# Kernel tuning notes

Hardware: AMD Instinct MI355X
Metric: run time of the kernel (lower is better)

Reference implementation:

```python
import jax, jax.numpy as jnp
import numpy as np

NUM_HEAD = 8   # in_channels // 64 for in_channels=512
DIM = 8        # per-head dim (== num_head in this module)
H_CH = NUM_HEAD * DIM  # 64
SCALE = DIM ** (-0.5)


def _conv(x, w, b, padding):
    # x: [N,C,H,W], w: [O,I,kh,kw]
    out = jax.lax.conv_general_dilated(
        x, w, window_strides=(1, 1), padding=padding,
        dimension_numbers=("NCHW", "OIHW", "NCHW"))
    return out + b[None, :, None, None]


def setup_inputs() -> dict:
    key = jax.random.key(0)
    ks = jax.random.split(key, 4)
    N, C, H, W = 4, 512, 48, 48
    x = jax.random.normal(ks[0], (N, C, H, W), dtype=jnp.float32)
    qkv_w = jax.random.normal(ks[1], (3 * H_CH, C, 1, 1), dtype=jnp.float32) * 0.05
    qkv_b = jnp.zeros((3 * H_CH,), dtype=jnp.float32)
    pos_w = jax.random.normal(ks[2], (H_CH, H_CH, 3, 3), dtype=jnp.float32) * 0.05
    pos_b = jnp.zeros((H_CH,), dtype=jnp.float32)
    res_w = jax.random.normal(ks[3], (C, H_CH, 1, 1), dtype=jnp.float32) * 0.05
    res_b = jnp.zeros((C,), dtype=jnp.float32)
    return {"x": x, "qkv_w": qkv_w, "qkv_b": qkv_b,
            "pos_w": pos_w, "pos_b": pos_b,
            "res_w": res_w, "res_b": res_b}


def reference(x, qkv_w, qkv_b, pos_w, pos_b, res_w, res_b):
    N, C, H, W = x.shape
    L = H * W
    # 1x1 conv QKV projection -> [N, 3h, H, W]
    qkv = _conv(x, qkv_w, qkv_b, "VALID")
    # [N, num_head, 3*dim, L]
    qkv = qkv.reshape(N, NUM_HEAD, 3 * DIM, L)
    q, k, v = qkv[:, :, :DIM], qkv[:, :, DIM:2 * DIM], qkv[:, :, 2 * DIM:]
    # attn = q^T @ k * scale : [N, nh, L, L], softmax over keys (last dim)
    attn = jnp.einsum("nhdq,nhdk->nhqk", q, k) * SCALE
    attn = jax.nn.softmax(attn, axis=-1)
    # out = v @ attn^T : [N, nh, dim, L]
    out = jnp.einsum("nhdk,nhqk->nhdq", v, attn)
    out = out.reshape(N, H_CH, H, W)
    # positional branch: 3x3 conv on v
    pos = _conv(v.reshape(N, H_CH, H, W), pos_w, pos_b, "SAME")
    out = out + pos
    # resume 1x1 conv -> [N, out_channels, H, W]
    return _conv(out, res_w, res_b, "VALID")
```

## Files before the change

kernel.cpp:

```cpp
#include <hip/hip_runtime.h>

#define L_ATT 2304
#define QSCALE_LOG2E 0.5100695712f

using bh8 = __attribute__((ext_vector_type(8))) short;
using f4  = __attribute__((ext_vector_type(4))) float;

#if __has_builtin(__builtin_amdgcn_exp2f)
#define EXP2(x) __builtin_amdgcn_exp2f(x)
#else
#define EXP2(x) exp2f(x)
#endif

__device__ inline short f2b(float f) {
    union { float f; unsigned u; } c; c.f = f;
    unsigned r = (c.u + 0x7FFFu + ((c.u >> 16) & 1u)) >> 16;
    return (short)r;
}
__device__ inline float b2f(short s) {
    union { unsigned u; float f; } c;
    c.u = ((unsigned)(unsigned short)s) << 16;
    return c.f;
}
__device__ inline int packhi(float lo, float hi) {
    return (int)__builtin_amdgcn_perm(__float_as_uint(hi), __float_as_uint(lo), 0x07060302u);
}

__global__ __launch_bounds__(256) void prep_kernel(
    const float* __restrict__ x, const float* __restrict__ qkv_w,
    const float* __restrict__ res_w, const float* __restrict__ pos_w,
    short* __restrict__ xt, short* __restrict__ wqb,
    short* __restrict__ reswb, short* __restrict__ wqp)
{
    __shared__ float s[64][68];
    const int g = blockIdx.x;
    if (g < 272) {
        int j = g * 256 + threadIdx.x;
        if (j < 24576) {
            float4 v = ((const float4*)qkv_w)[j];
            short4 o = { f2b(v.x), f2b(v.y), f2b(v.z), f2b(v.w) };
            *(short4*)(wqb + (size_t)j * 4) = o;
        } else if (j < 32768) {
            int idx = j - 24576;
            float4 v = ((const float4*)res_w)[idx];
            short4 o = { f2b(v.x), f2b(v.y), f2b(v.z), f2b(v.w) };
            *(short4*)(reswb + (size_t)idx * 4) = o;
        } else {
            int e = j - 32768;
            wqp[e] = f2b(pos_w[(size_t)(e & 4095) * 9 + (e >> 12)]);
        }
        return;
    }
    const int gg = g - 272;
    const int l0 = (gg % 36) * 64, k0 = ((gg / 36) & 7) * 64, n = gg / 288;
    const int tr = threadIdx.x >> 4, tc4 = (threadIdx.x & 15) * 4;
    const float* xp = x + ((size_t)n * 512 + k0) * L_ATT + l0;
#pragma unroll
    for (int r = 0; r < 4; ++r)
        *(float4*)&s[tr + r * 16][tc4] =
            *(const float4*)(xp + (size_t)(tr + r * 16) * L_ATT + tc4);
    __syncthreads();
    short* op = xt + ((size_t)n * L_ATT + l0) * 512 + k0;
#pragma unroll
    for (int r = 0; r < 4; ++r) {
        int l = tr + r * 16;
        short4 o = { f2b(s[tc4 + 0][l]), f2b(s[tc4 + 1][l]),
                     f2b(s[tc4 + 2][l]), f2b(s[tc4 + 3][l]) };
        *(short4*)(op + (size_t)l * 512 + tc4) = o;
    }
}

__global__ __launch_bounds__(256) void qkv_kernel(
    const short* __restrict__ xt, const short* __restrict__ wqb,
    const float* __restrict__ qkv_b, short* __restrict__ qt8,
    short* __restrict__ kt8, short* __restrict__ vt, short* __restrict__ vle)
{
    const int g = blockIdx.x;
    const int xcd = g & 7, rr = g >> 3;
    const int y = rr % 3, grp = rr / 3;
    const int code = grp * 8 + xcd;
    const int l0 = (code % 72) * 32, oc0 = y * 64, n = code / 72;

    const int lane = threadIdx.x & 63, wave = threadIdx.x >> 6;
    const int col = lane & 15, quad = lane >> 4;
    const int ocb = oc0 + wave * 16;

    f4 acc[2];
    acc[0] = (f4){0.f, 0.f, 0.f, 0.f};
    acc[1] = (f4){0.f, 0.f, 0.f, 0.f};

    const short* arow = wqb + (size_t)(ocb + col) * 512 + quad * 8;
    const short* brow = xt + ((size_t)n * L_ATT + l0 + col) * 512 + quad * 8;

#pragma unroll 4
    for (int k0 = 0; k0 < 512; k0 += 32) {
        bh8 af = *(const bh8*)(arow + k0);
        bh8 b0 = *(const bh8*)(brow + k0);
        bh8 b1 = *(const bh8*)(brow + (size_t)16 * 512 + k0);
        acc[0] = __builtin_amdgcn_mfma_f32_16x16x32_bf16(af, b0, acc[0], 0, 0, 0);
        acc[1] = __builtin_amdgcn_mfma_f32_16x16x32_bf16(af, b1, acc[1], 0, 0, 0);
    }

    const int obase = ocb + quad * 4;
    const int h = obase / 24;
    const int r0 = obase - h * 24;
    const int slice = n * 8 + h;

#pragma unroll
    for (int nt = 0; nt < 2; ++nt) {
        int l = l0 + nt * 16 + col;
        float v[4];
#pragma unroll
        for (int reg = 0; reg < 4; ++reg) v[reg] = acc[nt][reg] + qkv_b[obase + reg];
        if (r0 < 8) {
            short4 o = { f2b(v[0] * QSCALE_LOG2E), f2b(v[1] * QSCALE_LOG2E),
                         f2b(v[2] * QSCALE_LOG2E), f2b(v[3] * QSCALE_LOG2E) };
            *(short4*)(qt8 + ((size_t)slice * L_ATT + l) * 8 + r0) = o;
        } else if (r0 < 16) {
            short4 o = { f2b(v[0]), f2b(v[1]), f2b(v[2]), f2b(v[3]) };
            *(short4*)(kt8 + ((size_t)slice * L_ATT + l) * 8 + (r0 - 8)) = o;
        } else {
            short4 o = { f2b(v[0]), f2b(v[1]), f2b(v[2]), f2b(v[3]) };
            int d0 = r0 - 16;
#pragma unroll
            for (int reg = 0; reg < 4; ++reg)
                vt[((size_t)slice * 8 + d0 + reg) * L_ATT + l] = ((short*)&o)[reg];
            *(short4*)(vle + ((size_t)n * L_ATT + l) * 64 + h * 8 + d0) = o;
        }
    }
}

__global__ __launch_bounds__(256) void attnpos_kernel(
    const short* __restrict__ qt8, const short* __restrict__ kt8,
    const short* __restrict__ vt, const short* __restrict__ vle,
    const short* __restrict__ wqp, const float* __restrict__ pbias,
    float* __restrict__ pnum, float* __restrict__ pls, short* __restrict__ pcv)
{
    __shared__ short smem[4112];
    const int g = blockIdx.x;
    const int tid = threadIdx.x;
    const int lane = tid & 63, wave = tid >> 6;
    const int col = lane & 15, quad = lane >> 4;

    if (g < 1152) {
        const int h = g & 7, r = g >> 3;
        const int n = r / 36;
        const int rem = r - n * 36;
        const int qt = rem >> 1, half = rem & 1;
        const int q0 = qt * 128;
        const int kbase = half * 1152;
        const int slice = n * 8 + h;

        const short* qs  = qt8 + (size_t)slice * L_ATT * 8;
        const short* ks8 = kt8 + (size_t)slice * L_ATT * 8;
        const short* vb  = vt  + (size_t)slice * 8 * L_ATT;

        if (tid < 16) smem[4096 + tid] = (tid < 8) ? (short)0x3F80 : (short)0;

        bh8 zero8 = {0, 0, 0, 0, 0, 0, 0, 0};
        bh8 qf[2];
#pragma unroll
        for (int f = 0; f < 2; ++f) {
            qf[f] = zero8;
            if (quad == 0)
                qf[f] = *(const bh8*)(qs + (size_t)(q0 + wave * 32 + f * 16 + col) * 8);
        }

        int kidx[4];
#pragma unroll
        for (int nt = 0; nt < 4; ++nt)
            kidx[nt] = (quad == 0) ? (nt * 16 + col) * 8 : 4104;
        int vidx[2];
#pragma unroll
        for (int ks = 0; ks < 2; ++ks)
            vidx[ks] = (col < 8)
                     ? col * 64 + ((ks * 32 + quad * 8 + col * 8) & 63)
                     : ((col == 8) ? 4096 : 4104);

        const int ksl = ((lane >> 5) & 1) * 32 + ((lane >> 2) & 1) * 16
                      + ((lane >> 3) & 3) * 4 + (lane & 3);
        const int vd = lane >> 3, vkc = (lane & 7) * 8;
        const int vsl = vd * 64 + ((vkc + vd * 8) & 63);

        if (wave < 2)
            *(uint4*)&smem[wave * 512 + ksl * 8] =
                *(const uint4*)(ks8 + (size_t)(kbase + wave * 64 + lane) * 8);
        else
            *(uint4*)&smem[2048 + (wave - 2) * 512 + vsl] =
                *(const uint4*)(vb + (size_t)vd * L_ATT + kbase + (wave - 2) * 64 + vkc);
        __syncthreads();

        f4 oacc[2];
        oacc[0] = (f4){0.f, 0.f, 0.f, 0.f};
        oacc[1] = (f4){0.f, 0.f, 0.f, 0.f};

        int p = 0;
        for (int t = 0; t < 9; ++t) {
            uint4 dst;
            if (wave < 2)
                dst = *(const uint4*)(ks8 + (size_t)(kbase + (t * 2 + 2 + wave) * 64 + lane) * 8);
            else
                dst = *(const uint4*)(vb + (size_t)vd * L_ATT
                                      + kbase + (t * 2 + wave) * 64 + vkc);

#pragma unroll
            for (int u = 0; u < 2; ++u) {
                const int ku = (quad == 0) ? p * 1024 + u * 512 : 0;
                const int vu = (col < 8) ? 2048 + p * 1024 + u * 512 : 0;
                bh8 kf[4], vf[2];
#pragma unroll
                for (int nt = 0; nt < 4; ++nt) kf[nt] = *(const bh8*)&smem[kidx[nt] + ku];
#pragma unroll
                for (int ks = 0; ks < 2; ++ks) vf[ks] = *(const bh8*)&smem[vidx[ks] + vu];

                __builtin_amdgcn_s_setprio(1);
#pragma unroll
                for (int f = 0; f < 2; ++f) {
                    f4 s[4];
#pragma unroll
                    for (int nt = 0; nt < 4; ++nt) {
                        f4 z = (f4){0.f, 0.f, 0.f, 0.f};
                        s[nt] = __builtin_amdgcn_mfma_f32_16x16x32_bf16(kf[nt], qf[f], z, 0, 0, 0);
                    }
                    float e[4][4];
#pragma unroll
                    for (int nt = 0; nt < 4; ++nt)
#pragma unroll
                        for (int reg = 0; reg < 4; ++reg)
                            e[nt][reg] = EXP2(s[nt][reg]);
#pragma unroll
                    for (int ks = 0; ks < 2; ++ks) {
                        union { int i[4]; bh8 v; } pu;
                        pu.i[0] = packhi(e[2 * ks][0],     e[2 * ks][1]);
                        pu.i[1] = packhi(e[2 * ks][2],     e[2 * ks][3]);
                        pu.i[2] = packhi(e[2 * ks + 1][0], e[2 * ks + 1][1]);
                        pu.i[3] = packhi(e[2 * ks + 1][2], e[2 * ks + 1][3]);
                        oacc[f] = __builtin_amdgcn_mfma_f32_16x16x32_bf16(vf[ks], pu.v, oacc[f], 0, 0, 0);
                    }
                }
                __builtin_amdgcn_s_setprio(0);
            }

            if (wave < 2)
                *(uint4*)&smem[(p ^ 1) * 1024 + wave * 512 + ksl * 8] = dst;
            else
                *(uint4*)&smem[2048 + (p ^ 1) * 1024 + (wave - 2) * 512 + vsl] = dst;
            p ^= 1;
            __syncthreads();
        }

        const size_t prow = (size_t)(slice * 2 + half) * L_ATT;
#pragma unroll
        for (int f = 0; f < 2; ++f) {
            int qg = q0 + wave * 32 + f * 16 + col;
            if (quad < 2) {
                float4 o = { oacc[f][0], oacc[f][1], oacc[f][2], oacc[f][3] };
                *(float4*)(pnum + (prow + qg) * 8 + quad * 4) = o;
            } else if (quad == 2) {
                pls[prow + qg] = oacc[f][0];
            }
        }
        return;
    }

    const int gf = g - 1152;
    const int l0 = (gf % 144) * 16, n = gf / 144;
    const int t = wave;

    const int la = l0 + col;
    const int ya = la / 48, xa = la - ya * 48;

    f4 acc = (f4){0.f, 0.f, 0.f, 0.f};
    const short* vbase = vle + (size_t)n * L_ATT * 64;

#pragma unroll
    for (int q = 0; q < 9; ++q) {
        const int dy = q / 3 - 1, dx = q - (q / 3) * 3 - 1;
        const bool valid = ((unsigned)(ya + dy) < 48u) && ((unsigned)(xa + dx) < 48u);
        const short* ap = vbase + (size_t)(la + dy * 48 + dx) * 64 + quad * 8;
#pragma unroll
        for (int ks = 0; ks < 2; ++ks) {
            bh8 af = {0, 0, 0, 0, 0, 0, 0, 0};
            if (valid) af = *(const bh8*)(ap + ks * 32);
            bh8 bf = *(const bh8*)(wqp + ((size_t)q * 64 + t * 16 + col) * 64
                                   + ks * 32 + quad * 8);
            acc = __builtin_amdgcn_mfma_f32_16x16x32_bf16(af, bf, acc, 0, 0, 0);
        }
    }

    short* op = pcv + (size_t)n * L_ATT * 64;
    const int oc = t * 16 + col;
    const float bb = pbias[oc];
#pragma unroll
    for (int reg = 0; reg < 4; ++reg) {
        int l = l0 + quad * 4 + reg;
        op[(size_t)l * 64 + oc] = f2b(acc[reg] + bb);
    }
}

__global__ __launch_bounds__(256) void comb_kernel(
    const float* __restrict__ pnum, const float* __restrict__ pls,
    const short* __restrict__ pcv, short* __restrict__ battp)
{
    const int b = blockIdx.x;
    const int n = b / 144, lt = b % 144;
    const int hh = threadIdx.x & 15;
    const int l  = lt * 16 + (threadIdx.x >> 4);
    const int h = hh >> 1, dh = hh & 1;

    const size_t p0 = (size_t)((n * 8 + h) * 2) * L_ATT;
    const size_t p1 = p0 + L_ATT;
    float4 a = *(const float4*)(pnum + (p0 + l) * 8 + dh * 4);
    float4 c = *(const float4*)(pnum + (p1 + l) * 8 + dh * 4);
    float inv = 1.0f / (pls[p0 + l] + pls[p1 + l]);
    short4 pv = *(const short4*)(pcv + ((size_t)n * L_ATT + l) * 64 + hh * 4);

    int2 o;
    o.x = packhi((a.x + c.x) * inv + b2f(pv.x), (a.y + c.y) * inv + b2f(pv.y));
    o.y = packhi((a.z + c.z) * inv + b2f(pv.z), (a.w + c.w) * inv + b2f(pv.w));
    *(int2*)(battp + ((size_t)n * L_ATT + l) * 64 + hh * 4) = o;
}

__global__ __launch_bounds__(256) void res_kernel(
    const short* __restrict__ battp, const short* __restrict__ reswb,
    const float* __restrict__ res_b, float* __restrict__ out)
{
    const int g = blockIdx.x;
    const int xcd = g & 7, rr = g >> 3;
    const int y = rr & 7, grp = rr >> 3;
    const int code = grp * 8 + xcd;
    const int l0 = (code % 36) * 64, oc0 = y * 64, n = code / 36;

    const int lane = threadIdx.x & 63, wave = threadIdx.x >> 6;
    const int col = lane & 15, quad = lane >> 4;
    const int ocb = oc0 + wave * 16;

    f4 acc[4];
#pragma unroll
    for (int nt = 0; nt < 4; ++nt) acc[nt] = (f4){0.f, 0.f, 0.f, 0.f};

#pragma unroll
    for (int ks = 0; ks < 2; ++ks) {
        bh8 af = *(const bh8*)(reswb + (size_t)(ocb + col) * 64 + ks * 32 + quad * 8);
        const int ch = ks * 32 + quad * 8;
#pragma unroll
        for (int nt = 0; nt < 4; ++nt) {
            const int l = l0 + nt * 16 + col;
            bh8 bf = *(const bh8*)(battp + ((size_t)n * L_ATT + l) * 64 + ch);
            acc[nt] = __builtin_amdgcn_mfma_f32_16x16x32_bf16(af, bf, acc[nt], 0, 0, 0);
        }
    }

#pragma unroll
    for (int nt = 0; nt < 4; ++nt) {
        int l = l0 + nt * 16 + col;
#pragma unroll
        for (int reg = 0; reg < 4; ++reg) {
            int oc = ocb + quad * 4 + reg;
            out[((size_t)n * 512 + oc) * L_ATT + l] = acc[nt][reg] + res_b[oc];
        }
    }
}

extern "C" void kernel_launch(void* const* d_in, const int* in_sizes, int n_in,
                              void* d_out, int out_size, void* d_ws, size_t ws_size,
                              hipStream_t stream)
{
    const float* x      = (const float*)d_in[0];
    const float* qkv_w  = (const float*)d_in[1];
    const float* qkv_b  = (const float*)d_in[2];
    const float* pos_w  = (const float*)d_in[3];
    const float* pos_b  = (const float*)d_in[4];
    const float* res_w  = (const float*)d_in[5];
    const float* res_b  = (const float*)d_in[6];
    float* out = (float*)d_out;

    char* ws = (char*)d_ws;
    short* xt    = (short*)(ws);
    float* pnum  = (float*)(ws);
    float* pls   = (float*)(ws + 4718592);
    short* qt8   = (short*)(ws + 9437184);
    short* kt8   = (short*)(ws + 10616832);
    short* vt    = (short*)(ws + 11796480);
    short* pcv   = (short*)(ws + 12976128);
    short* wqb   = (short*)(ws + 14155776);
    short* reswb = (short*)(ws + 14352384);
    short* vle   = (short*)(ws + 14417920);
    short* wqp   = (short*)(ws + 15597568);
    short* battp = (short*)(ws + 15671296);

    prep_kernel<<<1424, 256, 0, stream>>>(x, qkv_w, res_w, pos_w, xt, wqb, reswb, wqp);
    qkv_kernel<<<864, 256, 0, stream>>>(xt, wqb, qkv_b, qt8, kt8, vt, vle);
    attnpos_kernel<<<1728, 256, 0, stream>>>(qt8, kt8, vt, vle, wqp, pos_b, pnum, pls, pcv);
    comb_kernel<<<576, 256, 0, stream>>>(pnum, pls, pcv, battp);
    res_kernel<<<1152, 256, 0, stream>>>(battp, reswb, res_b, out);
}
```

Measured before the change: 148.8 us.

## Stage X tile in LDS for QKV GEMM and deepen attention K/V pipeline stages

The QKV projection now copies the 32-row bf16 X tile into padded shared memory once per block instead of each wave re-reading it from global memory. The attention kernel processes three 64-key chunks per double-buffered stage instead of two, halving-ish the number of barriers and loop iterations while growing LDS usage. More LDS per block may reduce occupancy, and load balancing across waves for K/V prefetch becomes uneven.

```diff
diff --git a/kernel.cpp b/kernel.cpp
--- a/kernel.cpp
+++ b/kernel.cpp
@@ -75,28 +75,43 @@
     const float* __restrict__ qkv_b, short* __restrict__ qt8,
     short* __restrict__ kt8, short* __restrict__ vt, short* __restrict__ vle)
 {
+    __shared__ short bs[32 * 520];
     const int g = blockIdx.x;
     const int xcd = g & 7, rr = g >> 3;
     const int y = rr % 3, grp = rr / 3;
     const int code = grp * 8 + xcd;
     const int l0 = (code % 72) * 32, oc0 = y * 64, n = code / 72;
 
-    const int lane = threadIdx.x & 63, wave = threadIdx.x >> 6;
+    const int tid = threadIdx.x;
+    const int lane = tid & 63, wave = tid >> 6;
     const int col = lane & 15, quad = lane >> 4;
     const int ocb = oc0 + wave * 16;
+
+    {
+        const short* src = xt + ((size_t)n * L_ATT + l0) * 512;
+#pragma unroll
+        for (int j = 0; j < 8; ++j) {
+            int e = j * 256 + tid;
+            int row = e >> 6, c16 = e & 63;
+            uint4 v = *(const uint4*)(src + (size_t)row * 512 + c16 * 8);
+            *(uint4*)&bs[row * 520 + c16 * 8] = v;
+        }
+    }
+    __syncthreads();
 
     f4 acc[2];
     acc[0] = (f4){0.f, 0.f, 0.f, 0.f};
     acc[1] = (f4){0.f, 0.f, 0.f, 0.f};
 
     const short* arow = wqb + (size_t)(ocb + col) * 512 + quad * 8;
-    const short* brow = xt + ((size_t)n * L_ATT + l0 + col) * 512 + quad * 8;
+    const short* b0p = bs + col * 520 + quad * 8;
+    const short* b1p = b0p + 16 * 520;
 
 #pragma unroll 4
     for (int k0 = 0; k0 < 512; k0 += 32) {
         bh8 af = *(const bh8*)(arow + k0);
-        bh8 b0 = *(const bh8*)(brow + k0);
-        bh8 b1 = *(const bh8*)(brow + (size_t)16 * 512 + k0);
+        bh8 b0 = *(const bh8*)(b0p + k0);
+        bh8 b1 = *(const bh8*)(b1p + k0);
         acc[0] = __builtin_amdgcn_mfma_f32_16x16x32_bf16(af, b0, acc[0], 0, 0, 0);
         acc[1] = __builtin_amdgcn_mfma_f32_16x16x32_bf16(af, b1, acc[1], 0, 0, 0);
     }
@@ -136,7 +151,7 @@
     const short* __restrict__ wqp, const float* __restrict__ pbias,
     float* __restrict__ pnum, float* __restrict__ pls, short* __restrict__ pcv)
 {
-    __shared__ short smem[4112];
+    __shared__ short smem[6160];
     const int g = blockIdx.x;
     const int tid = threadIdx.x;
     const int lane = tid & 63, wave = tid >> 6;
@@ -155,7 +170,7 @@
         const short* ks8 = kt8 + (size_t)slice * L_ATT * 8;
         const short* vb  = vt  + (size_t)slice * 8 * L_ATT;
 
-        if (tid < 16) smem[4096 + tid] = (tid < 8) ? (short)0x3F80 : (short)0;
+        if (tid < 16) smem[6144 + tid] = (tid < 8) ? (short)0x3F80 : (short)0;
 
         bh8 zero8 = {0, 0, 0, 0, 0, 0, 0, 0};
         bh8 qf[2];
@@ -169,25 +184,31 @@
         int kidx[4];
 #pragma unroll
         for (int nt = 0; nt < 4; ++nt)
-            kidx[nt] = (quad == 0) ? (nt * 16 + col) * 8 : 4104;
+            kidx[nt] = (quad == 0) ? (nt * 16 + col) * 8 : 6152;
         int vidx[2];
 #pragma unroll
         for (int ks = 0; ks < 2; ++ks)
             vidx[ks] = (col < 8)
                      ? col * 64 + ((ks * 32 + quad * 8 + col * 8) & 63)
-                     : ((col == 8) ? 4096 : 4104);
+                     : ((col == 8) ? 6144 : 6152);
 
         const int ksl = ((lane >> 5) & 1) * 32 + ((lane >> 2) & 1) * 16
                       + ((lane >> 3) & 3) * 4 + (lane & 3);
         const int vd = lane >> 3, vkc = (lane & 7) * 8;
         const int vsl = vd * 64 + ((vkc + vd * 8) & 63);
 
-        if (wave < 2)
+        if (wave < 3)
             *(uint4*)&smem[wave * 512 + ksl * 8] =
                 *(const uint4*)(ks8 + (size_t)(kbase + wave * 64 + lane) * 8);
         else
-            *(uint4*)&smem[2048 + (wave - 2) * 512 + vsl] =
-                *(const uint4*)(vb + (size_t)vd * L_ATT + kbase + (wave - 2) * 64 + vkc);
+            *(uint4*)&smem[3072 + vsl] =
+                *(const uint4*)(vb + (size_t)vd * L_ATT + kbase + vkc);
+        if (wave == 0)
+            *(uint4*)&smem[3072 + 512 + vsl] =
+                *(const uint4*)(vb + (size_t)vd * L_ATT + kbase + 64 + vkc);
+        else if (wave == 1)
+            *(uint4*)&smem[3072 + 1024 + vsl] =
+                *(const uint4*)(vb + (size_t)vd * L_ATT + kbase + 128 + vkc);
         __syncthreads();
 
         f4 oacc[2];
@@ -195,18 +216,21 @@
         oacc[1] = (f4){0.f, 0.f, 0.f, 0.f};
 
         int p = 0;
-        for (int t = 0; t < 9; ++t) {
-            uint4 dst;
-            if (wave < 2)
-                dst = *(const uint4*)(ks8 + (size_t)(kbase + (t * 2 + 2 + wave) * 64 + lane) * 8);
+        for (int t = 0; t < 6; ++t) {
+            uint4 dA, dB;
+            if (wave < 3)
+                dA = *(const uint4*)(ks8 + (size_t)(kbase + (t * 3 + 3 + wave) * 64 + lane) * 8);
             else
-                dst = *(const uint4*)(vb + (size_t)vd * L_ATT
-                                      + kbase + (t * 2 + wave) * 64 + vkc);
-
-#pragma unroll
-            for (int u = 0; u < 2; ++u) {
-                const int ku = (quad == 0) ? p * 1024 + u * 512 : 0;
-                const int vu = (col < 8) ? 2048 + p * 1024 + u * 512 : 0;
+                dA = *(const uint4*)(vb + (size_t)vd * L_ATT + kbase + (t * 3 + 3) * 64 + vkc);
+            if (wave == 0)
+                dB = *(const uint4*)(vb + (size_t)vd * L_ATT + kbase + (t * 3 + 4) * 64 + vkc);
+            else if (wave == 1)
+                dB = *(const uint4*)(vb + (size_t)vd * L_ATT + kbase + (t * 3 + 5) * 64 + vkc);
+
+#pragma unroll
+            for (int u = 0; u < 3; ++u) {
+                const int ku = (quad == 0) ? p * 1536 + u * 512 : 0;
+                const int vu = (col < 8) ? 3072 + p * 1536 + u * 512 : 0;
                 bh8 kf[4], vf[2];
 #pragma unroll
                 for (int nt = 0; nt < 4; ++nt) kf[nt] = *(const bh8*)&smem[kidx[nt] + ku];
@@ -241,10 +265,14 @@
                 __builtin_amdgcn_s_setprio(0);
             }
 
-            if (wave < 2)
-                *(uint4*)&smem[(p ^ 1) * 1024 + wave * 512 + ksl * 8] = dst;
+            if (wave < 3)
+                *(uint4*)&smem[(p ^ 1) * 1536 + wave * 512 + ksl * 8] = dA;
             else
-                *(uint4*)&smem[2048 + (p ^ 1) * 1024 + (wave - 2) * 512 + vsl] = dst;
+                *(uint4*)&smem[3072 + (p ^ 1) * 1536 + vsl] = dA;
+            if (wave == 0)
+                *(uint4*)&smem[3072 + (p ^ 1) * 1536 + 512 + vsl] = dB;
+            else if (wave == 1)
+                *(uint4*)&smem[3072 + (p ^ 1) * 1536 + 1024 + vsl] = dB;
             p ^= 1;
             __syncthreads();
         }
```

New measurement: 135.8 us. 8.8% less time.
